# Optimization experiments

Hardware: AMD Instinct MI355X
Metric: run time of the kernel (lower is better)

Reference implementation:

```python
import math
import jax, jax.numpy as jnp
import numpy as np


def _bilinear_maps_sample(kv_feats, shapes_wh, start_ids, locs, map_ids):
    """Bilinear sampling from concatenated multi-level 2D maps.

    kv_feats: [BH, S, C] flattened (row-major, per level) feature maps
    shapes_wh: [L, 2] int (W, H) per level
    start_ids: [L] int start offset of each level in S
    locs: [BH, M, 2] normalized (x, y) in [0, 1]
    map_ids: [BH, M] int level index per sample
    returns [BH, M, C]
    """
    wh = shapes_wh[map_ids]                      # [BH, M, 2]
    W = wh[..., 0]
    H = wh[..., 1]
    start = start_ids[map_ids]                   # [BH, M]
    Wf = W.astype(locs.dtype)
    Hf = H.astype(locs.dtype)
    x = locs[..., 0] * Wf - 0.5                  # align_corners=False convention
    y = locs[..., 1] * Hf - 0.5
    x0 = jnp.floor(x)
    y0 = jnp.floor(y)
    out = jnp.zeros(locs.shape[:-1] + (kv_feats.shape[-1],), kv_feats.dtype)
    for dx in (0, 1):
        for dy in (0, 1):
            xi = x0 + dx
            yi = y0 + dy
            w = (1.0 - jnp.abs(x - xi)) * (1.0 - jnp.abs(y - yi))
            valid = (xi >= 0) & (xi < Wf) & (yi >= 0) & (yi < Hf)
            xi_c = jnp.clip(xi, 0, Wf - 1).astype(jnp.int32)
            yi_c = jnp.clip(yi, 0, Hf - 1).astype(jnp.int32)
            idx = start + yi_c * W + xi_c        # [BH, M]
            f = jnp.take_along_axis(kv_feats, idx[..., None], axis=1)
            out = out + jnp.where(valid, w, 0.0)[..., None] * f
    return out


def setup_inputs() -> dict:
    key = jax.random.key(0)
    ks = jax.random.split(key, 10)
    B, N, L, Hh, P = 2, 2048, 5, 8, 4
    in_size, sample_size = 256, 256
    qk_size, value_size = 256, 256
    kv_size = qk_size + value_size

    shapes = np.array([[128, 128], [64, 64], [32, 32], [16, 16], [8, 8]], np.int32)  # (H, W)
    flat = (shapes[:, 0] * shapes[:, 1]).astype(np.int64)
    start = np.concatenate([[0], np.cumsum(flat)[:-1]]).astype(np.int32)
    S = int(flat.sum())  # 21824

    # sampling_offsets bias: canonical Deformable-DETR grid init
    thetas = np.arange(Hh, dtype=np.float32) * (2.0 * math.pi / Hh)
    grid = np.stack([np.cos(thetas), np.sin(thetas)], axis=1)
    grid = grid / np.abs(grid).max(axis=1, keepdims=True)
    grid = np.tile(grid.reshape(Hh, 1, 1, 2), (1, L, 1, 1))
    sizes = np.arange(1, P + 1, dtype=np.float32).reshape(1, 1, P, 1)
    b_off = (sizes * grid).reshape(-1)           # [H*L*P*2]

    def lin(k, out_d, in_d):
        return jax.random.normal(k, (out_d, in_d), jnp.float32) * (1.0 / math.sqrt(in_d))

    return {
        "in_feats": jax.random.normal(ks[0], (B, N, in_size), jnp.float32),
        "sample_priors": jax.random.uniform(ks[1], (B, N, L, 2), jnp.float32),
        "sample_feats": jax.random.normal(ks[2], (B, S, sample_size), jnp.float32),
        "sample_map_shapes": jnp.asarray(shapes),
        "sample_map_start_ids": jnp.asarray(start),
        "W_off": jax.random.normal(ks[3], (Hh * L * P * 2, in_size), jnp.float32) * 0.02,
        "b_off": jnp.asarray(b_off),
        "W_q": lin(ks[4], qk_size, in_size),
        "b_q": jnp.zeros((qk_size,), jnp.float32),
        "W_kv": lin(ks[5], kv_size, sample_size),
        "b_kv": jnp.zeros((kv_size,), jnp.float32),
        "point_encs": jax.random.normal(ks[6], (Hh, L * P, qk_size // Hh), jnp.float32) * 0.02,
        "W_out": lin(ks[7], in_size, value_size),
        "b_out": jnp.zeros((in_size,), jnp.float32),
    }


def reference(in_feats, sample_priors, sample_feats, sample_map_shapes,
              sample_map_start_ids, W_off, b_off, W_q, b_q, W_kv, b_kv,
              point_encs, W_out, b_out):
    B, N = in_feats.shape[:2]
    Hh, LP, dqk = point_encs.shape
    L = sample_map_shapes.shape[0]
    P = LP // L

    # sampling offsets + locations (priors last dim == 2 path)
    off = (in_feats @ W_off.T + b_off).reshape(B, N, Hh, L, P, 2)
    shapes_wh = sample_map_shapes[:, ::-1]                      # fliplr -> (W, H)
    norm = shapes_wh.astype(in_feats.dtype)[None, None, None, :, None, :]
    locs = sample_priors[:, :, None, :, None, :] + off / norm    # [B,N,H,L,P,2]

    q = (in_feats @ W_q.T + b_q).reshape(B, N, Hh, dqk)
    kv = sample_feats @ W_kv.T + b_kv                            # [B,S,kv_size]
    ck = kv.shape[-1] // Hh
    kv = kv.reshape(B, -1, Hh, ck).transpose(0, 2, 1, 3).reshape(B * Hh, -1, ck)

    locs = locs.transpose(0, 2, 1, 3, 4, 5).reshape(B * Hh, N * L * P, 2)
    map_ids = jnp.broadcast_to(jnp.arange(L, dtype=jnp.int32)[None, None, :, None],
                               (B * Hh, N, L, P)).reshape(B * Hh, -1)

    sampled = _bilinear_maps_sample(kv, shapes_wh, sample_map_start_ids, locs, map_ids)
    sampled = sampled.reshape(B, Hh, N, LP, ck).transpose(0, 2, 1, 3, 4)  # [B,N,H,LP,ck]

    keys = sampled[..., :dqk] + point_encs                       # [B,N,H,LP,dqk]
    vals = sampled[..., dqk:]                                    # [B,N,H,LP,cv]
    attn = jax.nn.softmax(
        jnp.einsum('bnhd,bnhpd->bnhp', q / math.sqrt(dqk), keys), axis=-1)
    weighted = jnp.einsum('bnhp,bnhpd->bnhd', attn, vals).reshape(B, N, -1)
    return weighted @ W_out.T + b_out
```

## Files before the change

kernel.cpp:

```cpp
#include <hip/hip_runtime.h>
#include <cstddef>

#define B_  2
#define N_  2048
#define L_  5
#define HH  8
#define P_  4
#define S_  21824
#define DQK 32

using bf16x8 = __attribute__((ext_vector_type(8))) short;
using f32x4  = __attribute__((ext_vector_type(4))) float;
using us8    = __attribute__((ext_vector_type(8))) unsigned short;

__device__ __forceinline__ unsigned short f2b(float f) {
  unsigned u = __builtin_bit_cast(unsigned, f);
  u += 0x7FFFu + ((u >> 16) & 1u);
  return (unsigned short)(u >> 16);
}
__device__ __forceinline__ float b2f(unsigned short h) {
  return __builtin_bit_cast(float, ((unsigned)h) << 16);
}
__device__ __forceinline__ unsigned cvtpk(float lo, float hi) {
  unsigned r;
  asm("v_cvt_pk_bf16_f32 %0, %1, %2" : "=v"(r) : "v"(lo), "v"(hi));
  return r;
}

__device__ __forceinline__ void gld_lds16(const void* g, void* l) {
  __builtin_amdgcn_global_load_lds(
      (const __attribute__((address_space(1))) unsigned int*)g,
      (__attribute__((address_space(3))) unsigned int*)l, 16, 0, 0);
}

template <int CTRL>
__device__ __forceinline__ float dppadd(float v) {
  const int x = __builtin_bit_cast(int, v);
  return v + __builtin_bit_cast(float,
      __builtin_amdgcn_update_dpp(x, x, CTRL, 0xF, 0xF, false));
}

#define F0 131072
#define F1 147456
#define F2 155648
#define F3 163840
#define F4 176128
#define F5 188416

__device__ __forceinline__ void cvt8_plain(const float* s, unsigned short* d, int u) {
  const float4 a = ((const float4*)s)[2 * u];
  const float4 b = ((const float4*)s)[2 * u + 1];
  us8 o;
  o[0] = f2b(a.x); o[1] = f2b(a.y); o[2] = f2b(a.z); o[3] = f2b(a.w);
  o[4] = f2b(b.x); o[5] = f2b(b.y); o[6] = f2b(b.z); o[7] = f2b(b.w);
  ((us8*)d)[u] = o;
}
__device__ __forceinline__ unsigned short f2b_lo(float x) {
  return f2b(x - b2f(f2b(x)));
}
__device__ __forceinline__ void cvt8_lo(const float* s, unsigned short* d, int u) {
  const float4 a = ((const float4*)s)[2 * u];
  const float4 b = ((const float4*)s)[2 * u + 1];
  us8 o;
  o[0] = f2b_lo(a.x); o[1] = f2b_lo(a.y); o[2] = f2b_lo(a.z); o[3] = f2b_lo(a.w);
  o[4] = f2b_lo(b.x); o[5] = f2b_lo(b.y); o[6] = f2b_lo(b.z); o[7] = f2b_lo(b.w);
  ((us8*)d)[u] = o;
}
__device__ __forceinline__ void cvt8_both(const float* s, unsigned short* dh,
                                          unsigned short* dl, int u) {
  const float4 a = ((const float4*)s)[2 * u];
  const float4 b = ((const float4*)s)[2 * u + 1];
  us8 oh, ol;
  const float v[8] = {a.x, a.y, a.z, a.w, b.x, b.y, b.z, b.w};
#pragma unroll
  for (int k = 0; k < 8; ++k) {
    const unsigned short h = f2b(v[k]);
    oh[k] = h;
    ol[k] = f2b(v[k] - b2f(h));
  }
  ((us8*)dh)[u] = oh;
  ((us8*)dl)[u] = ol;
}

__global__ __launch_bounds__(256) void cvt_all(
    const float* __restrict__ in_feats, const float* __restrict__ W_kv,
    const float* __restrict__ W_q, const float* __restrict__ W_out,
    const float* __restrict__ W_off,
    unsigned short* __restrict__ if_hi, unsigned short* __restrict__ if_lo,
    unsigned short* __restrict__ wkv_bf, unsigned short* __restrict__ wq_bf,
    unsigned short* __restrict__ wout_bf, unsigned short* __restrict__ woff_hi,
    unsigned short* __restrict__ woff_lo) {
  const int i = blockIdx.x * 256 + threadIdx.x;
  if      (i < F0) cvt8_both(in_feats, if_hi, if_lo, i);
  else if (i < F1) cvt8_plain(W_kv, wkv_bf, i - F0);
  else if (i < F2) cvt8_plain(W_q, wq_bf, i - F1);
  else if (i < F3) cvt8_plain(W_out, wout_bf, i - F2);
  else if (i < F4) {
    const int u = i - F3;
    if ((u >> 5) < 320) cvt8_plain(W_off, woff_hi, u);
    else ((us8*)woff_hi)[u] = (us8)0;
  } else {
    const int u = i - F4;
    if ((u >> 5) < 320) cvt8_lo(W_off, woff_lo, u);
    else ((us8*)woff_lo)[u] = (us8)0;
  }
}

__device__ __forceinline__ void mfma_compute(
    const unsigned short* As, const unsigned short* Bs,
    int wr, int wc, int fr, int fq, f32x4 (&acc)[4][4]) {
#pragma unroll
  for (int kk = 0; kk < 2; ++kk) {
    bf16x8 af[4], bfv[4];
#pragma unroll
    for (int i = 0; i < 4; ++i) {
      const int ar = wr * 64 + i * 16 + fr;
      const int cha = (kk * 4 + fq) ^ (ar & 7);
      af[i] = *(const bf16x8*)(As + ar * 64 + cha * 8);
      const int br = wc * 64 + i * 16 + fr;
      const int chb = (kk * 4 + fq) ^ (br & 7);
      bfv[i] = *(const bf16x8*)(Bs + br * 64 + chb * 8);
    }
#pragma unroll
    for (int i = 0; i < 4; ++i)
#pragma unroll
      for (int j = 0; j < 4; ++j)
        acc[i][j] = __builtin_amdgcn_mfma_f32_16x16x32_bf16(
            af[i], bfv[j], acc[i][j], 0, 0, 0);
  }
}

__device__ __forceinline__ void mfma_tile_bf16(
    const unsigned short* __restrict__ Ap, const unsigned short* __restrict__ Wp,
    unsigned short* As, unsigned short* Bs,
    int row0, int col0, int wv, int wr, int wc, int fr, int fq,
    int srow, int sch, f32x4 (&acc)[4][4]) {
  for (int k0 = 0; k0 < 256; k0 += 64) {
#pragma unroll
    for (int i = 0; i < 4; ++i) {
      const int r = i * 32 + srow;
      const int ca = sch ^ (r & 7);
      gld_lds16(Ap + (size_t)(row0 + r) * 256 + k0 + ca * 8,
                As + (size_t)(i * 32 + wv * 8) * 64);
      gld_lds16(Wp + (size_t)(col0 + r) * 256 + k0 + ca * 8,
                Bs + (size_t)(i * 32 + wv * 8) * 64);
    }
    __syncthreads();
    mfma_compute(As, Bs, wr, wc, fr, fq, acc);
    __syncthreads();
  }
}

__device__ __forceinline__ void mfma_tile_f32A(
    const float* __restrict__ Af, const unsigned short* __restrict__ Wp,
    unsigned short* As, unsigned short* Bs,
    int row0, int col0, int wv, int wr, int wc, int fr, int fq,
    int srow, int sch, int tid, f32x4 (&acc)[4][4]) {
  const int arow = tid >> 1;
  const int cb = (tid & 1) * 4;
  for (int k0 = 0; k0 < 256; k0 += 64) {
#pragma unroll
    for (int i = 0; i < 4; ++i) {
      const int r = i * 32 + srow;
      const int ca = sch ^ (r & 7);
      gld_lds16(Wp + (size_t)(col0 + r) * 256 + k0 + ca * 8,
                Bs + (size_t)(i * 32 + wv * 8) * 64);
    }
    const float* arp = Af + (size_t)(row0 + arow) * 256 + k0;
#pragma unroll
    for (int c = 0; c < 4; ++c) {
      const int ch = cb + c;
      const float4 a0 = *(const float4*)(arp + ch * 8);
      const float4 a1 = *(const float4*)(arp + ch * 8 + 4);
      uint4 u;
      u.x = cvtpk(a0.x, a0.y);
      u.y = cvtpk(a0.z, a0.w);
      u.z = cvtpk(a1.x, a1.y);
      u.w = cvtpk(a1.z, a1.w);
      *(uint4*)(As + arow * 64 + (ch ^ (arow & 7)) * 8) = u;
    }
    __syncthreads();
    mfma_compute(As, Bs, wr, wc, fr, fq, acc);
    __syncthreads();
  }
}

__global__ __launch_bounds__(256) void ubergemm(
    const float* __restrict__ sfeats,
    const unsigned short* __restrict__ wkv_bf,
    const unsigned short* __restrict__ if_hi,
    const unsigned short* __restrict__ if_lo,
    const unsigned short* __restrict__ woff_hi,
    const unsigned short* __restrict__ woff_lo,
    const unsigned short* __restrict__ wq_bf,
    const float* __restrict__ b_kv, const float* __restrict__ b_off,
    const float* __restrict__ b_q,
    unsigned short* __restrict__ kvt, float* __restrict__ offb,
    float* __restrict__ qb) {
  __shared__ __align__(16) unsigned short As[128 * 64];
  __shared__ __align__(16) unsigned short Bs[128 * 64];

  const int tid = threadIdx.x;
  const int lane = tid & 63;
  const int wv = tid >> 6;
  const int wr = wv >> 1, wc = wv & 1;
  const int fr = lane & 15, fq = lane >> 4;
  const int srow = tid >> 3;
  const int sch = tid & 7;
  const int bx = blockIdx.x;

  f32x4 acc[4][4] = {};
  int kvmode = 0, row0, col0, ldc = 0, nbias = 0;
  const float* bias;
  float* Cf = nullptr;

  if (bx < 96) {
    col0 = (bx % 3) * 128; row0 = (bx / 3) * 128;
    bias = b_off; Cf = offb; ldc = 384; nbias = 320;
    mfma_tile_bf16(if_hi, woff_hi, As, Bs, row0, col0, wv, wr, wc, fr, fq, srow, sch, acc);
    mfma_tile_bf16(if_hi, woff_lo, As, Bs, row0, col0, wv, wr, wc, fr, fq, srow, sch, acc);
    mfma_tile_bf16(if_lo, woff_hi, As, Bs, row0, col0, wv, wr, wc, fr, fq, srow, sch, acc);
  } else if (bx < 160) {
    const int t = bx - 96;
    col0 = (t & 1) * 128; row0 = (t >> 1) * 128;
    bias = b_q; Cf = qb; ldc = 256; nbias = 256;
    mfma_tile_bf16(if_hi, wq_bf, As, Bs, row0, col0, wv, wr, wc, fr, fq, srow, sch, acc);
  } else {
    const int t = bx - 160;
    int row, col;
    if (t < 1344) {
      const int x = t & 7;
      const int s2 = t >> 3;
      col = s2 & 3;
      row = (s2 >> 2) * 8 + x;
    } else {
      const int u2 = t - 1344;
      row = 336 + (u2 >> 2);
      col = u2 & 3;
    }
    row0 = row * 128; col0 = col * 128;
    kvmode = 1; bias = b_kv;
    mfma_tile_f32A(sfeats, wkv_bf, As, Bs, row0, col0, wv, wr, wc, fr, fq, srow, sch, tid, acc);
  }

#pragma unroll
  for (int j = 0; j < 4; ++j) {
    const int n = col0 + wc * 64 + j * 16 + fr;
    const float bv = kvmode ? bias[n] : ((n < nbias) ? bias[n] : 0.f);
#pragma unroll
    for (int i = 0; i < 4; ++i) {
      const int mbase = row0 + wr * 64 + i * 16 + fq * 4;
#pragma unroll
      for (int r = 0; r < 4; ++r) {
        const int m = mbase + r;
        if (kvmode) {
          const int b = (m >= S_) ? 1 : 0;
          const int s = m - b * S_;
          const int h = n >> 6, c = n & 63;
          kvt[((size_t)(b * HH + h) * S_ + s) * 64 + c] = f2b(acc[i][j][r] + bv);
        } else {
          Cf[(size_t)m * ldc + n] = acc[i][j][r] + bv;
        }
      }
    }
  }
}

__global__ __launch_bounds__(256) void gemm_out(
    const unsigned short* __restrict__ A, const unsigned short* __restrict__ Wt,
    const float* __restrict__ bias, float* __restrict__ C) {
  __shared__ __align__(16) unsigned short As[128 * 64];
  __shared__ __align__(16) unsigned short Bs[128 * 64];
  const int tid = threadIdx.x;
  const int lane = tid & 63;
  const int wv = tid >> 6;
  const int wr = wv >> 1, wc = wv & 1;
  const int fr = lane & 15, fq = lane >> 4;
  const int row0 = blockIdx.y * 128, col0 = blockIdx.x * 128;
  const int srow = tid >> 3, sch = tid & 7;
  f32x4 acc[4][4] = {};
  mfma_tile_bf16(A, Wt, As, Bs, row0, col0, wv, wr, wc, fr, fq, srow, sch, acc);
#pragma unroll
  for (int j = 0; j < 4; ++j) {
    const int n = col0 + wc * 64 + j * 16 + fr;
    const float bv = bias[n];
#pragma unroll
    for (int i = 0; i < 4; ++i) {
      const int mbase = row0 + wr * 64 + i * 16 + fq * 4;
#pragma unroll
      for (int r = 0; r < 4; ++r)
        C[(size_t)(mbase + r) * 256 + n] = acc[i][j][r] + bv;
    }
  }
}

__global__ __launch_bounds__(256) void sample_attn4(
    const unsigned short* __restrict__ kvt,
    const float* __restrict__ offb,
    const float* __restrict__ qb,
    const float* __restrict__ priors,
    const int* __restrict__ shapes,
    const int* __restrict__ starts,
    const float* __restrict__ pencs,
    unsigned short* __restrict__ wtd) {
  __shared__ __align__(16) int pbuf[4][20][8];
  const int wv = threadIdx.x >> 6;
  const int lane = threadIdx.x & 63;
  const int beta = blockIdx.x;
  const int sig = (beta & 7) * 2 + ((beta >> 3) & 1);
  const int chunk = beta >> 4;
  const int h = sig & 7;
  const int b = sig >> 3;
  const int bn = b * N_ + chunk * 4 + wv;
  const int j = lane & 31;
  const int half = lane >> 5;

  if (lane < 20) {
    const int pp = lane;
    const int l = pp >> 2;
    const float2 oxy = *(const float2*)(offb + (size_t)bn * 384 + h * 40 + pp * 2);
    const float2 pxy = *(const float2*)(priors + ((size_t)bn * 5 + l) * 2);
    const int Wd = shapes[l * 2 + 1];
    const int Hd = shapes[l * 2 + 0];
    const int st = starts[l];
    const float Wf = (float)Wd, Hf = (float)Hd;
    const float x = (pxy.x + oxy.x / Wf) * Wf - 0.5f;
    const float y = (pxy.y + oxy.y / Hf) * Hf - 0.5f;
    const float x0f = floorf(x), y0f = floorf(y);
    const float fx = x - x0f, fy = y - y0f;
    const int xi = (int)x0f, yi = (int)y0f;
    int a[4]; float w[4];
#pragma unroll
    for (int dy = 0; dy < 2; ++dy)
#pragma unroll
      for (int dx = 0; dx < 2; ++dx) {
        const int xc = xi + dx, yc = yi + dy;
        const bool valid = (xc >= 0) & (xc < Wd) & (yc >= 0) & (yc < Hd);
        const float wt = (dx ? fx : 1.f - fx) * (dy ? fy : 1.f - fy);
        const int xcc = min(max(xc, 0), Wd - 1);
        const int ycc = min(max(yc, 0), Hd - 1);
        a[dy * 2 + dx] = (st + ycc * Wd + xcc) * 32;
        w[dy * 2 + dx] = valid ? wt : 0.f;
      }
    *(int4*)&pbuf[wv][pp][0] = make_int4(a[0], a[1], a[2], a[3]);
    *(float4*)&pbuf[wv][pp][4] = make_float4(w[0], w[1], w[2], w[3]);
  }

  const int jc = j & 15;
  float2 q2 = *(const float2*)(qb + (size_t)bn * 256 + h * DQK + 2 * jc);
  q2.x *= 0.17677669529663687f;
  q2.y *= 0.17677669529663687f;
  float qpe[10];
#pragma unroll
  for (int i = 0; i < 10; ++i) {
    const float2 pe = *(const float2*)(
        pencs + ((size_t)h * 20 + 2 * i + half) * DQK + 2 * jc);
    qpe[i] = q2.x * pe.x + q2.y * pe.y;
  }

  const unsigned* kvd = (const unsigned*)(kvt + (size_t)(b * HH + h) * (S_ * 64));
  int4 aa[2]; float4 ww[2]; unsigned g[2][4];
  aa[0] = *(const int4*)&pbuf[wv][half][0];
  ww[0] = *(const float4*)&pbuf[wv][half][4];
  g[0][0] = kvd[(unsigned)aa[0].x + j];
  g[0][1] = kvd[(unsigned)aa[0].y + j];
  g[0][2] = kvd[(unsigned)aa[0].z + j];
  g[0][3] = kvd[(unsigned)aa[0].w + j];

  float2 sam[10];
  float lg[10];
#pragma unroll
  for (int i = 0; i < 10; ++i) {
    const int cur = i & 1, nxt = cur ^ 1;
    if (i < 9) {
      aa[nxt] = *(const int4*)&pbuf[wv][2 * (i + 1) + half][0];
      ww[nxt] = *(const float4*)&pbuf[wv][2 * (i + 1) + half][4];
      g[nxt][0] = kvd[(unsigned)aa[nxt].x + j];
      g[nxt][1] = kvd[(unsigned)aa[nxt].y + j];
      g[nxt][2] = kvd[(unsigned)aa[nxt].z + j];
      g[nxt][3] = kvd[(unsigned)aa[nxt].w + j];
    }
    const float4 wt = ww[cur];
    const unsigned g0 = g[cur][0], g1 = g[cur][1], g2 = g[cur][2], g3 = g[cur][3];
    const float lo0 = __builtin_bit_cast(float, g0 << 16);
    const float hi0 = __builtin_bit_cast(float, g0 & 0xFFFF0000u);
    const float lo1 = __builtin_bit_cast(float, g1 << 16);
    const float hi1 = __builtin_bit_cast(float, g1 & 0xFFFF0000u);
    const float lo2 = __builtin_bit_cast(float, g2 << 16);
    const float hi2 = __builtin_bit_cast(float, g2 & 0xFFFF0000u);
    const float lo3 = __builtin_bit_cast(float, g3 << 16);
    const float hi3 = __builtin_bit_cast(float, g3 & 0xFFFF0000u);
    float vx = wt.x * lo0;  vx = fmaf(wt.y, lo1, vx);
    vx = fmaf(wt.z, lo2, vx); vx = fmaf(wt.w, lo3, vx);
    float vy = wt.x * hi0;  vy = fmaf(wt.y, hi1, vy);
    vy = fmaf(wt.z, hi2, vy); vy = fmaf(wt.w, hi3, vy);
    sam[i].x = vx; sam[i].y = vy;
    float part = (j < 16) ? fmaf(q2.x, vx, fmaf(q2.y, vy, qpe[i])) : 0.f;
    part = dppadd<0xB1>(part);
    part = dppadd<0x4E>(part);
    part = dppadd<0x124>(part);
    part = dppadd<0x128>(part);
    lg[i] = part + __shfl_xor(part, 16, 64);
  }

  float mx = lg[0];
#pragma unroll
  for (int i = 1; i < 10; ++i) mx = fmaxf(mx, lg[i]);
  mx = fmaxf(mx, __shfl_xor(mx, 32, 64));
  float se = 0.f;
#pragma unroll
  for (int i = 0; i < 10; ++i) {
    lg[i] = __expf(lg[i] - mx);
    se += lg[i];
  }
  se += __shfl_xor(se, 32, 64);
  const float inv = 1.f / se;

  float ax = 0.f, ay = 0.f;
#pragma unroll
  for (int i = 0; i < 10; ++i) {
    ax = fmaf(lg[i], sam[i].x, ax);
    ay = fmaf(lg[i], sam[i].y, ay);
  }
  ax += __shfl_xor(ax, 32, 64);
  ay += __shfl_xor(ay, 32, 64);

  if (half == 0 && j >= 16) {
    const unsigned u = (unsigned)f2b(ax * inv) | ((unsigned)f2b(ay * inv) << 16);
    ((unsigned*)wtd)[(size_t)bn * 128 + h * 16 + (j - 16)] = u;
  }
}

extern "C" void kernel_launch(void* const* d_in, const int* in_sizes, int n_in,
                              void* d_out, int out_size, void* d_ws, size_t ws_size,
                              hipStream_t stream) {
  const float* in_feats = (const float*)d_in[0];
  const float* priors   = (const float*)d_in[1];
  const float* sfeats   = (const float*)d_in[2];
  const int*   shapes   = (const int*)d_in[3];
  const int*   starts   = (const int*)d_in[4];
  const float* W_off    = (const float*)d_in[5];
  const float* b_off    = (const float*)d_in[6];
  const float* W_q      = (const float*)d_in[7];
  const float* b_q      = (const float*)d_in[8];
  const float* W_kv     = (const float*)d_in[9];
  const float* b_kv     = (const float*)d_in[10];
  const float* pencs    = (const float*)d_in[11];
  const float* W_out    = (const float*)d_in[12];
  const float* b_out    = (const float*)d_in[13];
  float* out = (float*)d_out;

  char* w = (char*)d_ws;
  unsigned short* kvt = (unsigned short*)w;
  w += (size_t)B_ * HH * S_ * 64 * 2;
  unsigned short* if_hi = (unsigned short*)w; w += (size_t)4096 * 256 * 2;
  unsigned short* if_lo = (unsigned short*)w; w += (size_t)4096 * 256 * 2;
  unsigned short* wkv_bf = (unsigned short*)w;  w += (size_t)512 * 256 * 2;
  unsigned short* wq_bf  = (unsigned short*)w;  w += (size_t)256 * 256 * 2;
  unsigned short* wout_bf = (unsigned short*)w; w += (size_t)256 * 256 * 2;
  unsigned short* woff_hi = (unsigned short*)w; w += (size_t)384 * 256 * 2;
  unsigned short* woff_lo = (unsigned short*)w; w += (size_t)384 * 256 * 2;
  float* offb = (float*)w;  w += (size_t)4096 * 384 * 4;
  float* qb   = (float*)w;  w += (size_t)4096 * 256 * 4;
  unsigned short* wtd_bf = (unsigned short*)w; w += (size_t)4096 * 256 * 2;

  cvt_all<<<F5 / 256, 256, 0, stream>>>(
      in_feats, W_kv, W_q, W_out, W_off,
      if_hi, if_lo, wkv_bf, wq_bf, wout_bf, woff_hi, woff_lo);

  ubergemm<<<1524, 256, 0, stream>>>(
      sfeats, wkv_bf, if_hi, if_lo, woff_hi, woff_lo, wq_bf,
      b_kv, b_off, b_q, kvt, offb, qb);

  sample_attn4<<<(B_ * N_ * HH) / 4, 256, 0, stream>>>(
      kvt, offb, qb, priors, shapes, starts, pencs, wtd_bf);

  gemm_out<<<dim3(2, 32), 256, 0, stream>>>(wtd_bf, wout_bf, b_out, out);
}
```

Before: 101.6 us.

## Keep full-K W_kv tile resident in LDS and stream fp32 A into registers

```diff
diff --git a/kernel.cpp b/kernel.cpp
--- a/kernel.cpp
+++ b/kernel.cpp
@@ -151,40 +151,6 @@
   }
 }
 
-__device__ __forceinline__ void mfma_tile_f32A(
-    const float* __restrict__ Af, const unsigned short* __restrict__ Wp,
-    unsigned short* As, unsigned short* Bs,
-    int row0, int col0, int wv, int wr, int wc, int fr, int fq,
-    int srow, int sch, int tid, f32x4 (&acc)[4][4]) {
-  const int arow = tid >> 1;
-  const int cb = (tid & 1) * 4;
-  for (int k0 = 0; k0 < 256; k0 += 64) {
-#pragma unroll
-    for (int i = 0; i < 4; ++i) {
-      const int r = i * 32 + srow;
-      const int ca = sch ^ (r & 7);
-      gld_lds16(Wp + (size_t)(col0 + r) * 256 + k0 + ca * 8,
-                Bs + (size_t)(i * 32 + wv * 8) * 64);
-    }
-    const float* arp = Af + (size_t)(row0 + arow) * 256 + k0;
-#pragma unroll
-    for (int c = 0; c < 4; ++c) {
-      const int ch = cb + c;
-      const float4 a0 = *(const float4*)(arp + ch * 8);
-      const float4 a1 = *(const float4*)(arp + ch * 8 + 4);
-      uint4 u;
-      u.x = cvtpk(a0.x, a0.y);
-      u.y = cvtpk(a0.z, a0.w);
-      u.z = cvtpk(a1.x, a1.y);
-      u.w = cvtpk(a1.z, a1.w);
-      *(uint4*)(As + arow * 64 + (ch ^ (arow & 7)) * 8) = u;
-    }
-    __syncthreads();
-    mfma_compute(As, Bs, wr, wc, fr, fq, acc);
-    __syncthreads();
-  }
-}
-
 __global__ __launch_bounds__(256) void ubergemm(
     const float* __restrict__ sfeats,
     const unsigned short* __restrict__ wkv_bf,
@@ -197,71 +163,117 @@
     const float* __restrict__ b_q,
     unsigned short* __restrict__ kvt, float* __restrict__ offb,
     float* __restrict__ qb) {
-  __shared__ __align__(16) unsigned short As[128 * 64];
-  __shared__ __align__(16) unsigned short Bs[128 * 64];
+  __shared__ __align__(16) unsigned short lds[128 * 256];
 
   const int tid = threadIdx.x;
   const int lane = tid & 63;
   const int wv = tid >> 6;
   const int wr = wv >> 1, wc = wv & 1;
   const int fr = lane & 15, fq = lane >> 4;
+  const int bx = blockIdx.x;
+
+  f32x4 acc[4][4] = {};
+
+  if (bx >= 160) {
+    const int t = bx - 160;
+    const int x = t & 7;
+    const int idx = t >> 3;
+    const int c = idx & 3;
+    const int gi = idx >> 2;
+    const int g = gi * 8 + x;
+    if (g >= 341) return;
+    const int row0 = g * 128;
+    const int col0 = c * 128;
+
+#pragma unroll
+    for (int s = 0; s < 16; ++s) {
+      const int ci = s * 256 + tid;
+      const int n = ci >> 5, cc = ci & 31;
+      gld_lds16(wkv_bf + (size_t)(col0 + n) * 256 + (cc ^ (n & 7)) * 8,
+                lds + (s * 256 + wv * 64) * 8);
+    }
+    __syncthreads();
+
+#pragma unroll 2
+    for (int kk = 0; kk < 8; ++kk) {
+      bf16x8 af[4], bfv[4];
+#pragma unroll
+      for (int i = 0; i < 4; ++i) {
+        const float* ap = sfeats +
+            (size_t)(row0 + wr * 64 + i * 16 + fr) * 256 + kk * 32 + fq * 8;
+        const float4 a0 = *(const float4*)ap;
+        const float4 a1 = *(const float4*)(ap + 4);
+        uint4 u;
+        u.x = cvtpk(a0.x, a0.y);
+        u.y = cvtpk(a0.z, a0.w);
+        u.z = cvtpk(a1.x, a1.y);
+        u.w = cvtpk(a1.z, a1.w);
+        af[i] = __builtin_bit_cast(bf16x8, u);
+      }
+#pragma unroll
+      for (int j = 0; j < 4; ++j) {
+        const int n = wc * 64 + j * 16 + fr;
+        const int ch = (kk * 4 + fq) ^ (n & 7);
+        bfv[j] = *(const bf16x8*)(lds + (n * 32 + ch) * 8);
+      }
+#pragma unroll
+      for (int i = 0; i < 4; ++i)
+#pragma unroll
+        for (int j = 0; j < 4; ++j)
+          acc[i][j] = __builtin_amdgcn_mfma_f32_16x16x32_bf16(
+              af[i], bfv[j], acc[i][j], 0, 0, 0);
+    }
+
+#pragma unroll
+    for (int j = 0; j < 4; ++j) {
+      const int n = col0 + wc * 64 + j * 16 + fr;
+      const float bv = b_kv[n];
+      const int h = n >> 6, cch = n & 63;
+#pragma unroll
+      for (int i = 0; i < 4; ++i) {
+        const int mbase = row0 + wr * 64 + i * 16 + fq * 4;
+#pragma unroll
+        for (int r = 0; r < 4; ++r) {
+          const int m = mbase + r;
+          const int b = (m >= S_) ? 1 : 0;
+          const int s = m - b * S_;
+          kvt[((size_t)(b * HH + h) * S_ + s) * 64 + cch] = f2b(acc[i][j][r] + bv);
+        }
+      }
+    }
+    return;
+  }
+
+  unsigned short* As = lds;
+  unsigned short* Bs = lds + 128 * 64;
   const int srow = tid >> 3;
   const int sch = tid & 7;
-  const int bx = blockIdx.x;
-
-  f32x4 acc[4][4] = {};
-  int kvmode = 0, row0, col0, ldc = 0, nbias = 0;
+  int row0, col0, ldc, nbias;
   const float* bias;
-  float* Cf = nullptr;
-
+  float* Cf;
   if (bx < 96) {
     col0 = (bx % 3) * 128; row0 = (bx / 3) * 128;
     bias = b_off; Cf = offb; ldc = 384; nbias = 320;
     mfma_tile_bf16(if_hi, woff_hi, As, Bs, row0, col0, wv, wr, wc, fr, fq, srow, sch, acc);
     mfma_tile_bf16(if_hi, woff_lo, As, Bs, row0, col0, wv, wr, wc, fr, fq, srow, sch, acc);
     mfma_tile_bf16(if_lo, woff_hi, As, Bs, row0, col0, wv, wr, wc, fr, fq, srow, sch, acc);
-  } else if (bx < 160) {
+  } else {
     const int t = bx - 96;
     col0 = (t & 1) * 128; row0 = (t >> 1) * 128;
     bias = b_q; Cf = qb; ldc = 256; nbias = 256;
     mfma_tile_bf16(if_hi, wq_bf, As, Bs, row0, col0, wv, wr, wc, fr, fq, srow, sch, acc);
-  } else {
-    const int t = bx - 160;
-    int row, col;
-    if (t < 1344) {
-      const int x = t & 7;
-      const int s2 = t >> 3;
-      col = s2 & 3;
-      row = (s2 >> 2) * 8 + x;
-    } else {
-      const int u2 = t - 1344;
-      row = 336 + (u2 >> 2);
-      col = u2 & 3;
-    }
-    row0 = row * 128; col0 = col * 128;
-    kvmode = 1; bias = b_kv;
-    mfma_tile_f32A(sfeats, wkv_bf, As, Bs, row0, col0, wv, wr, wc, fr, fq, srow, sch, tid, acc);
   }
 
 #pragma unroll
   for (int j = 0; j < 4; ++j) {
     const int n = col0 + wc * 64 + j * 16 + fr;
-    const float bv = kvmode ? bias[n] : ((n < nbias) ? bias[n] : 0.f);
+    const float bv = (n < nbias) ? bias[n] : 0.f;
 #pragma unroll
     for (int i = 0; i < 4; ++i) {
       const int mbase = row0 + wr * 64 + i * 16 + fq * 4;
 #pragma unroll
-      for (int r = 0; r < 4; ++r) {
-        const int m = mbase + r;
-        if (kvmode) {
-          const int b = (m >= S_) ? 1 : 0;
-          const int s = m - b * S_;
-          const int h = n >> 6, c = n & 63;
-          kvt[((size_t)(b * HH + h) * S_ + s) * 64 + c] = f2b(acc[i][j][r] + bv);
-        } else {
-          Cf[(size_t)m * ldc + n] = acc[i][j][r] + bv;
-        }
-      }
+      for (int r = 0; r < 4; ++r)
+        Cf[(size_t)(mbase + r) * ldc + n] = acc[i][j][r] + bv;
     }
   }
 }
@@ -468,7 +480,7 @@
       in_feats, W_kv, W_q, W_out, W_off,
       if_hi, if_lo, wkv_bf, wq_bf, wout_bf, woff_hi, woff_lo);
 
-  ubergemm<<<1524, 256, 0, stream>>>(
+  ubergemm<<<1536, 256, 0, stream>>>(
       sfeats, wkv_bf, if_hi, if_lo, woff_hi, woff_lo, wq_bf,
       b_kv, b_off, b_q, kvt, offb, qb);
 
```

New measurement: 102.3 us. No clear change (+0.7%).
